# Kernel optimization log

Measured on AMD Instinct MI355X. Metric: run time of the kernel, lower is better.

## Reference

```python
import jax, jax.numpy as jnp
import numpy as np

DEGREE = 3


def bspline_basis(t, knots, degree):
    """Vectorized Cox-de Boor recursion. t: [S], knots: [K]. Returns B: [S, K-degree-1].
    Faithful to the torch loop: at degree d only columns [0, n_knots-d) are updated;
    higher columns keep their stale lower-degree values, and term2 reads the
    not-yet-updated column i+1 (i.e. previous-degree values), matching ascending-i
    in-place updates.
    """
    n_knots = knots.shape[0] - degree - 1
    # degree-0 basis: indicator of half-open knot spans
    B = ((knots[None, :n_knots] <= t[:, None]) &
         (t[:, None] < knots[None, 1:n_knots + 1])).astype(t.dtype)
    for d in range(1, degree + 1):
        n = n_knots - d
        denom1 = knots[d:d + n] - knots[:n]          # knots[i+d]   - knots[i]
        denom2 = knots[d + 1:d + 1 + n] - knots[1:1 + n]  # knots[i+d+1] - knots[i+1]
        safe1 = jnp.where(denom1 == 0, 1.0, denom1)
        safe2 = jnp.where(denom2 == 0, 1.0, denom2)
        w1 = jnp.where(denom1 == 0, 0.0, (t[:, None] - knots[None, :n]) / safe1)
        w2 = jnp.where(denom2 == 0, 0.0, (knots[None, d + 1:d + 1 + n] - t[:, None]) / safe2)
        new_cols = w1 * B[:, :n] + w2 * B[:, 1:n + 1]
        B = B.at[:, :n].set(new_cols)
    return B


def setup_inputs() -> dict:
    key = jax.random.key(0)
    k1, k2 = jax.random.split(key)
    N_KNOTS, DIM, T_MAX = 2048, 512, 32768.0
    t = jnp.sort(jax.random.uniform(k1, (N_KNOTS,), dtype=jnp.float32)) * T_MAX
    t = t.at[-1].set(T_MAX)  # make sample range exactly [0, T_MAX)
    c = jax.random.normal(k2, (DIM, N_KNOTS), dtype=jnp.float32)
    return {"t": t, "c": c, "delta": 1}


def reference(t, c, delta):
    padded_t = jnp.concatenate([jnp.zeros(DEGREE + 1, dtype=t.dtype), t])
    # number of samples is data-dependent (t[-1]); concretize outside jit
    t_max = float(t[-1])
    sample_points = jnp.arange(0.0, t_max, float(delta), dtype=t.dtype)  # [S]
    B = bspline_basis(sample_points, padded_t, DEGREE)  # [S, n_knots]
    spline_values = B @ c.T  # [S, dim]
    return sample_points, spline_values
```

## Files before the change

kernel.cpp:

```cpp
#include <hip/hip_runtime.h>


#define DEG 3
#define SBLK 64
#define DBLK 256
#define NCOLS 32
#define CSTRIDE (DBLK + 4)

typedef float vfloat4 __attribute__((ext_vector_type(4)));

__device__ __forceinline__ float kn(const float* __restrict__ t, int i) {
    return (i < DEG + 1) ? 0.0f : t[i - (DEG + 1)];
}

__global__ __launch_bounds__(256) void bspline_fused(
    const float* __restrict__ t, const float* __restrict__ c,
    const int* __restrict__ delta_p, float* __restrict__ out_pts,
    vfloat4* __restrict__ out_spline, int S, int NK, int DIM, int nd, int nwg)
{
    __shared__ __attribute__((aligned(16))) float lc[NCOLS][CSTRIDE];
    __shared__ vfloat4 bwS[SBLK];
    __shared__ int jS[SBLK];

    const int tid = threadIdx.x;
    const int bid = blockIdx.x;
    const int L = (bid & 7) * (nwg >> 3) + (bid >> 3);
    const int dchunk = L & (nd - 1);
    const int sb = L >> 1;
    const int s0 = sb * SBLK;
    const int dbase = dchunk * DBLK;

    if (tid < SBLK) {
        const int s = s0 + tid;
        const int sc = (s < S) ? s : (S - 1);
        const float delta = (float)(*delta_p);
        const float sv = (float)sc * delta;
        if (dchunk == 0 && s < S) out_pts[s] = sv;

        int lo = DEG, hi = NK + DEG - 1;
        while (lo < hi) {
            int mid = (lo + hi + 1) >> 1;
            if (kn(t, mid) <= sv) lo = mid; else hi = mid - 1;
        }
        int j = lo;
        vfloat4 b4 = (vfloat4){0.f, 0.f, 0.f, 0.f};
        if (j < NK) {
            float N[DEG + 1][DEG + 1];
            N[0][0] = 1.0f;
            #pragma unroll
            for (int d = 1; d <= DEG; ++d) {
                #pragma unroll
                for (int k = 0; k <= d; ++k) {
                    int i = j - d + k;
                    float vpi  = (k >= 1) ? N[d - 1][k - 1] : 0.0f;
                    float vpi1 = (k <= d - 1) ? N[d - 1][k] : 0.0f;
                    float ki   = kn(t, i);
                    float kid  = kn(t, i + d);
                    float ki1  = kn(t, i + 1);
                    float kid1 = kn(t, i + d + 1);
                    float den1 = kid - ki;
                    float den2 = kid1 - ki1;
                    float w1 = (den1 != 0.0f) ? (sv - ki) / den1 : 0.0f;
                    float w2 = (den2 != 0.0f) ? (kid1 - sv) / den2 : 0.0f;
                    N[d][k] = w1 * vpi + w2 * vpi1;
                }
            }
            float b[DEG + 1];
            #pragma unroll
            for (int m = 0; m <= DEG; ++m) {
                int col = j - DEG + m;
                int deg = NK - 1 - col; if (deg > DEG) deg = DEG;
                int idx = m - DEG + deg;
                b[m] = (idx >= 0) ? N[deg][idx] : 0.0f;
            }
            b4 = (vfloat4){b[0], b[1], b[2], b[3]};
        } else {
            j = NK - 1;
        }
        jS[tid] = j;
        bwS[tid] = b4;
    }
    __syncthreads();

    const int colmin = jS[0] - DEG;
    int nc = jS[SBLK - 1] - colmin + 1;
    if (nc > NCOLS) nc = NCOLS;
    int ncr = 8, lsh = 3;
    while (ncr < nc) { ncr <<= 1; ++lsh; }
    for (int e = tid; e < ncr * DBLK; e += 256) {
        int cc = e & (ncr - 1);
        int dd = e >> lsh;
        int col = colmin + cc;
        if (col > NK - 1) col = NK - 1;
        lc[cc][dd] = c[(size_t)(dbase + dd) * NK + col];
    }
    __syncthreads();

    const int nv = DIM >> 2;
    vfloat4* ob = out_spline + (size_t)s0 * nv + (dbase >> 2);
    #pragma unroll
    for (int k = 0; k < (SBLK * (DBLK >> 2)) / 256; ++k) {
        const int it = k * 256 + tid;
        const int sl = it >> 6;
        const int d4 = it & 63;
        const int j = jS[sl];
        const vfloat4 b = bwS[sl];
        const int cl = j - DEG - colmin;
        vfloat4 r;
        if (cl + DEG < NCOLS) {
            const float* p = &lc[cl][d4 << 2];
            vfloat4 a0 = *(const vfloat4*)(p);
            vfloat4 a1 = *(const vfloat4*)(p + CSTRIDE);
            vfloat4 a2 = *(const vfloat4*)(p + 2 * CSTRIDE);
            vfloat4 a3 = *(const vfloat4*)(p + 3 * CSTRIDE);
            r = b.x * a0 + b.y * a1 + b.z * a2 + b.w * a3;
        } else {
            float rv[4];
            #pragma unroll
            for (int q = 0; q < 4; ++q) {
                const float* cq = c + (size_t)(dbase + (d4 << 2) + q) * NK + (j - DEG);
                rv[q] = b.x * cq[0] + b.y * cq[1] + b.z * cq[2] + b.w * cq[3];
            }
            r = (vfloat4){rv[0], rv[1], rv[2], rv[3]};
        }
        if (s0 + sl < S)
            ob[(size_t)sl * nv + d4] = r;
    }
}

extern "C" void kernel_launch(void* const* d_in, const int* in_sizes, int n_in,
                              void* d_out, int out_size, void* d_ws, size_t ws_size,
                              hipStream_t stream) {
    const float* t = (const float*)d_in[0];
    const float* c = (const float*)d_in[1];
    const int* delta = (const int*)d_in[2];
    const int NK = in_sizes[0];
    const int DIM = in_sizes[1] / NK;
    const int S = out_size / (1 + DIM);

    const int nd = DIM / DBLK;
    const int nsb = (S + SBLK - 1) / SBLK;
    const int nwg = nsb * nd;
    bspline_fused<<<nwg, 256, 0, stream>>>(
        t, c, delta, (float*)d_out,
        (vfloat4*)((float*)d_out + S), S, NK, DIM, nd, nwg);
}
```

Baseline: 88.19 us.

## Prefetch fixed 16-column coefficient window before basis computation, drop per-sample binary search

```diff
diff --git a/kernel.cpp b/kernel.cpp
--- a/kernel.cpp
+++ b/kernel.cpp
@@ -4,7 +4,7 @@
 #define DEG 3
 #define SBLK 64
 #define DBLK 256
-#define NCOLS 32
+#define NSTAGE 16
 #define CSTRIDE (DBLK + 4)
 
 typedef float vfloat4 __attribute__((ext_vector_type(4)));
@@ -18,31 +18,49 @@
     const int* __restrict__ delta_p, float* __restrict__ out_pts,
     vfloat4* __restrict__ out_spline, int S, int NK, int DIM, int nd, int nwg)
 {
-    __shared__ __attribute__((aligned(16))) float lc[NCOLS][CSTRIDE];
+    __shared__ __attribute__((aligned(16))) float lc[NSTAGE][CSTRIDE];
     __shared__ vfloat4 bwS[SBLK];
     __shared__ int jS[SBLK];
 
     const int tid = threadIdx.x;
     const int bid = blockIdx.x;
     const int L = (bid & 7) * (nwg >> 3) + (bid >> 3);
-    const int dchunk = L & (nd - 1);
-    const int sb = L >> 1;
+    const int dchunk = L % nd;
+    const int sb = L / nd;
     const int s0 = sb * SBLK;
     const int dbase = dchunk * DBLK;
+
+    const float delta = (float)(*delta_p);
+
+    const float sv0 = (float)s0 * delta;
+    int lo = DEG, hi = NK + DEG - 1;
+    while (lo < hi) {
+        int mid = (lo + hi + 1) >> 1;
+        if (kn(t, mid) <= sv0) lo = mid; else hi = mid - 1;
+    }
+    const int j0 = lo;
+
+    int cmin4 = (j0 - DEG) & ~3;
+    if (cmin4 > NK - NSTAGE) cmin4 = NK - NSTAGE;
+
+    const int c4 = tid & 3;
+    const int dd0 = tid >> 2;
+    vfloat4 st[4];
+    #pragma unroll
+    for (int i = 0; i < 4; ++i) {
+        const int dd = dd0 + 64 * i;
+        st[i] = *(const vfloat4*)(c + (size_t)(dbase + dd) * NK + cmin4 + 4 * c4);
+    }
 
     if (tid < SBLK) {
         const int s = s0 + tid;
         const int sc = (s < S) ? s : (S - 1);
-        const float delta = (float)(*delta_p);
         const float sv = (float)sc * delta;
         if (dchunk == 0 && s < S) out_pts[s] = sv;
 
-        int lo = DEG, hi = NK + DEG - 1;
-        while (lo < hi) {
-            int mid = (lo + hi + 1) >> 1;
-            if (kn(t, mid) <= sv) lo = mid; else hi = mid - 1;
-        }
-        int j = lo;
+        int j = j0;
+        while (j < NK + DEG - 1 && kn(t, j + 1) <= sv) ++j;
+
         vfloat4 b4 = (vfloat4){0.f, 0.f, 0.f, 0.f};
         if (j < NK) {
             float N[DEG + 1][DEG + 1];
@@ -80,19 +98,13 @@
         jS[tid] = j;
         bwS[tid] = b4;
     }
-    __syncthreads();
 
-    const int colmin = jS[0] - DEG;
-    int nc = jS[SBLK - 1] - colmin + 1;
-    if (nc > NCOLS) nc = NCOLS;
-    int ncr = 8, lsh = 3;
-    while (ncr < nc) { ncr <<= 1; ++lsh; }
-    for (int e = tid; e < ncr * DBLK; e += 256) {
-        int cc = e & (ncr - 1);
-        int dd = e >> lsh;
-        int col = colmin + cc;
-        if (col > NK - 1) col = NK - 1;
-        lc[cc][dd] = c[(size_t)(dbase + dd) * NK + col];
+    #pragma unroll
+    for (int i = 0; i < 4; ++i) {
+        const int dd = dd0 + 64 * i;
+        #pragma unroll
+        for (int q = 0; q < 4; ++q)
+            lc[4 * c4 + q][dd] = st[i][q];
     }
     __syncthreads();
 
@@ -105,9 +117,9 @@
         const int d4 = it & 63;
         const int j = jS[sl];
         const vfloat4 b = bwS[sl];
-        const int cl = j - DEG - colmin;
+        const int cl = j - DEG - cmin4;
         vfloat4 r;
-        if (cl + DEG < NCOLS) {
+        if (cl + DEG < NSTAGE) {
             const float* p = &lc[cl][d4 << 2];
             vfloat4 a0 = *(const vfloat4*)(p);
             vfloat4 a1 = *(const vfloat4*)(p + CSTRIDE);
```

After: 88.05 us. Within noise of the previous version (-0.2%).
